# Kernel optimization log

Hardware: AMD Instinct MI355X
Metric: run time of the kernel (lower is better)

## Reference

```python
import jax, jax.numpy as jnp
import numpy as np

B, N, C, H = 4, 4096, 512, 16  # batch, seq (=input_resolution), dim, num_heads


def setup_inputs() -> dict:
    key = jax.random.key(0)
    k1, k2, k3, k4 = jax.random.split(key, 4)
    x = jax.random.normal(k1, (B, N, C), jnp.float32)
    Wqk = jax.random.normal(k2, (C, 2 * C), jnp.float32) / np.sqrt(C)
    bqk = jnp.zeros((2 * C,), jnp.float32)
    lepe_w = jax.random.normal(k3, (C, 1, 3), jnp.float32) * 0.1  # depthwise conv, groups=C
    lepe_b = jnp.zeros((C,), jnp.float32)
    return {"x": x, "Wqk": Wqk, "bqk": bqk, "lepe_w": lepe_w, "lepe_b": lepe_b}


def _rope(x):
    # x: [b, n, c]; 1D RoPE over the sequence axis, k_max = c // 2 pairs.
    b, n, c = x.shape
    k_max = c // 2
    theta = 1.0 / (10000.0 ** (jnp.arange(k_max, dtype=jnp.float32) / k_max))
    ang = jnp.arange(n, dtype=jnp.float32)[:, None] * theta  # [n, k_max]
    cos, sin = jnp.cos(ang), jnp.sin(ang)
    xr, xi = x[..., 0::2], x[..., 1::2]  # consecutive (re, im) pairs
    out = jnp.stack([xr * cos - xi * sin, xr * sin + xi * cos], axis=-1)
    return out.reshape(b, n, c)


def reference(x, Wqk, bqk, lepe_w, lepe_b):
    b, n, c = x.shape
    h = H
    d = c // h
    qk = x @ Wqk + bqk  # [b, n, 2c]
    q = jax.nn.elu(qk[..., :c]) + 1.0
    k = jax.nn.elu(qk[..., c:]) + 1.0
    q_rope = _rope(q).reshape(b, n, h, d).transpose(0, 2, 1, 3)  # [b,h,n,d]
    k_rope = _rope(k).reshape(b, n, h, d).transpose(0, 2, 1, 3)
    qh = q.reshape(b, n, h, d).transpose(0, 2, 1, 3)
    kh = k.reshape(b, n, h, d).transpose(0, 2, 1, 3)
    v = x.reshape(b, n, h, d).transpose(0, 2, 1, 3)
    # normalizer z = 1 / (q . mean_n(k) + eps)
    kmean = kh.mean(axis=2)  # [b,h,d]
    z = 1.0 / (jnp.einsum('bhnd,bhd->bhn', qh, kmean) + 1e-6)  # [b,h,n]
    # kv = (k_rope^T / sqrt(n)) @ (v / sqrt(n))
    kv = jnp.einsum('bhnd,bhne->bhde', k_rope, v) / n  # [b,h,d,d]
    out = jnp.einsum('bhnd,bhde->bhne', q_rope, kv) * z[..., None]  # [b,h,n,d]
    out = out.transpose(0, 2, 1, 3).reshape(b, n, c)
    # LePE: depthwise conv1d over sequence on v (v reassembled == x)
    vt = x.transpose(0, 2, 1)  # [b, c, n]
    lepe = jax.lax.conv_general_dilated(
        vt, lepe_w, window_strides=(1,), padding=((1, 1),),
        feature_group_count=c, dimension_numbers=('NCH', 'OIH', 'NCH'))
    lepe = lepe + lepe_b[None, :, None]
    return out + lepe.transpose(0, 2, 1)
```

## Files before the change

kernel.cpp:

```cpp
#include <hip/hip_runtime.h>

typedef unsigned short u16;
typedef u16   u16x8 __attribute__((ext_vector_type(8)));
typedef short s16x8 __attribute__((ext_vector_type(8)));
typedef float f32x4 __attribute__((ext_vector_type(4)));

__device__ __forceinline__ float b2f(u16 u) {
    return __uint_as_float(((unsigned)u) << 16);
}
__device__ __forceinline__ u16 f2b(float f) {
    unsigned x = __float_as_uint(f);
    x += 0x7fffu + ((x >> 16) & 1u);
    return (u16)(x >> 16);
}
__device__ __forceinline__ void gload_lds(const u16* g, u16* l) {
    __builtin_amdgcn_global_load_lds(
        (const __attribute__((address_space(1))) unsigned int*)g,
        (__attribute__((address_space(3))) unsigned int*)l, 16, 0, 0);
}

#define THETA_SCALE 0.05190512648261f

__global__ __launch_bounds__(256)
void k_prep(const float* __restrict__ X, u16* __restrict__ Xb,
            const float* __restrict__ W, u16* __restrict__ WT,
            float* __restrict__ kvz) {
    if (blockIdx.x < 4096) {
        size_t i = (size_t)(blockIdx.x * 256 + threadIdx.x) * 8;
        float4 a = *(const float4*)(X + i);
        float4 b = *(const float4*)(X + i + 4);
        u16x8 r;
        r[0] = f2b(a.x); r[1] = f2b(a.y); r[2] = f2b(a.z); r[3] = f2b(a.w);
        r[4] = f2b(b.x); r[5] = f2b(b.y); r[6] = f2b(b.z); r[7] = f2b(b.w);
        *(u16x8*)(Xb + i) = r;
    } else if (blockIdx.x < 4608) {
        __shared__ float tile[32][33];
        int bid = blockIdx.x - 4096;
        int c0 = (bid & 31) * 32;
        int r0 = (bid >> 5) * 32;
        int tx = threadIdx.x & 31;
        int ty = threadIdx.x >> 5;
        #pragma unroll
        for (int i = 0; i < 4; ++i) {
            int r = ty + i * 8;
            tile[r][tx] = W[(size_t)(r0 + r) * 1024 + c0 + tx];
        }
        __syncthreads();
        #pragma unroll
        for (int i = 0; i < 4; ++i) {
            int r = ty + i * 8;
            WT[(size_t)(c0 + r) * 512 + r0 + tx] = f2b(tile[tx][r]);
        }
    } else {
        size_t i = (size_t)(blockIdx.x - 4608) * 1024 + threadIdx.x * 4;
        *(float4*)(kvz + i) = make_float4(0.f, 0.f, 0.f, 0.f);
    }
}

__global__ __launch_bounds__(256)
void k_gemm(const u16* __restrict__ Xb, const u16* __restrict__ WT,
            const float* __restrict__ bqk,
            u16* __restrict__ Qb, u16* __restrict__ Kb) {
    __shared__ u16 As[128 * 64];
    __shared__ u16 Bs[128 * 64];
    const int t = threadIdx.x;
    const int m0 = blockIdx.x * 128;
    const int n0 = blockIdx.y * 128;
    const int lane = t & 63;
    const int wave = t >> 6;
    const int wm = (wave >> 1) * 64;
    const int wn = (wave & 1) * 64;
    const int quad = lane >> 4;
    const int l16 = lane & 15;
    const int lr = lane >> 3;
    const int cg = ((lane & 7) ^ lr) * 8;

    f32x4 acc[4][4];
    f32x4 zero4 = {0.f, 0.f, 0.f, 0.f};
    #pragma unroll
    for (int i = 0; i < 4; ++i)
        #pragma unroll
        for (int j = 0; j < 4; ++j) acc[i][j] = zero4;

    for (int k0 = 0; k0 < 512; k0 += 64) {
        __syncthreads();
        #pragma unroll
        for (int g = 0; g < 4; ++g) {
            int r0 = wave * 32 + g * 8;
            size_t ga = (size_t)(m0 + r0 + lr) * 512 + k0 + cg;
            size_t gb = (size_t)(n0 + r0 + lr) * 512 + k0 + cg;
            gload_lds(Xb + ga, &As[r0 * 64]);
            gload_lds(WT + gb, &Bs[r0 * 64]);
        }
        __syncthreads();
        #pragma unroll
        for (int ks = 0; ks < 64; ks += 32) {
            const int cbase = quad + (ks >> 3);
            s16x8 a4[4], b4[4];
            #pragma unroll
            for (int i = 0; i < 4; ++i) {
                int row = wm + i * 16 + l16;
                a4[i] = *(const s16x8*)&As[row * 64 + ((cbase ^ (row & 7)) * 8)];
            }
            #pragma unroll
            for (int j = 0; j < 4; ++j) {
                int row = wn + j * 16 + l16;
                b4[j] = *(const s16x8*)&Bs[row * 64 + ((cbase ^ (row & 7)) * 8)];
            }
            #pragma unroll
            for (int i = 0; i < 4; ++i)
                #pragma unroll
                for (int j = 0; j < 4; ++j)
                    acc[i][j] = __builtin_amdgcn_mfma_f32_16x16x32_bf16(
                        a4[i], b4[j], acc[i][j], 0, 0, 0);
        }
    }

    u16* O = (n0 < 512) ? Qb : Kb;
    #pragma unroll
    for (int i = 0; i < 4; ++i)
        #pragma unroll
        for (int j = 0; j < 4; ++j) {
            int col = n0 + wn + j * 16 + l16;
            float bias = bqk[col];
            int gc = col & 511;
            #pragma unroll
            for (int r = 0; r < 4; ++r) {
                int grow = m0 + wm + i * 16 + quad * 4 + r;
                float v = acc[i][j][r] + bias;
                v = v > 0.f ? v + 1.f : __expf(v);
                O[(size_t)grow * 512 + gc] = f2b(v);
            }
        }
}

__global__ __launch_bounds__(256)
void k_kv(const u16* __restrict__ Kb, const u16* __restrict__ Xb,
          float* __restrict__ kvbuf, float* __restrict__ ksum) {
    const int bh = blockIdx.x;
    const int b = bh >> 4, h = bh & 15;
    const int nb = blockIdx.y * 512;
    __shared__ u16 krT[32 * 72];
    __shared__ u16 vT[32 * 72];
    __shared__ float red[64 * 36];
    const int t = threadIdx.x;
    const int row = t >> 2;
    const int c8 = (t & 3) * 8;
    const int rot_w = 16 * ((c8 >> 3) & 3);
    const int lane = t & 63;
    const int wave = t >> 6;
    const int quad = lane >> 4;
    const int l16 = lane & 15;
    const int dq = (wave >> 1) * 16;
    const int eq = (wave & 1) * 16;
    const int ca = dq + l16;
    const int cb2 = eq + l16;
    const int rot_a = 16 * ((ca >> 3) & 3);
    const int rot_b = 16 * ((cb2 >> 3) & 3);

    float ksl[8] = {0, 0, 0, 0, 0, 0, 0, 0};
    f32x4 acc = {0.f, 0.f, 0.f, 0.f};

    float th[4];
    #pragma unroll
    for (int p = 0; p < 4; ++p)
        th[p] = exp2f(-THETA_SCALE * (float)(h * 16 + (c8 >> 1) + p));

    for (int pass = 0; pass < 8; ++pass) {
        int n = nb + pass * 64 + row;
        size_t base = (size_t)(b * 4096 + n) * 512 + h * 32 + c8;
        u16x8 k8 = *(const u16x8*)(Kb + base);
        u16x8 v8 = *(const u16x8*)(Xb + base);
        float kf[8], kr[8];
        #pragma unroll
        for (int j = 0; j < 8; ++j) kf[j] = b2f(k8[j]);
        #pragma unroll
        for (int p = 0; p < 4; ++p) {
            float sv, cv;
            sincosf((float)n * th[p], &sv, &cv);
            kr[2 * p]     = kf[2 * p] * cv - kf[2 * p + 1] * sv;
            kr[2 * p + 1] = kf[2 * p] * sv + kf[2 * p + 1] * cv;
        }
        #pragma unroll
        for (int j = 0; j < 8; ++j) ksl[j] += kf[j];
        if (pass) __syncthreads();
        int colw = (row + rot_w) & 63;
        #pragma unroll
        for (int j = 0; j < 8; ++j) {
            krT[(c8 + j) * 72 + colw] = f2b(kr[j]);
            vT[(c8 + j) * 72 + colw] = v8[j];
        }
        __syncthreads();
        #pragma unroll
        for (int ks = 0; ks < 64; ks += 32) {
            s16x8 a4 = *(const s16x8*)&krT[ca * 72 + ((ks + quad * 8 + rot_a) & 63)];
            s16x8 b4 = *(const s16x8*)&vT[cb2 * 72 + ((ks + quad * 8 + rot_b) & 63)];
            acc = __builtin_amdgcn_mfma_f32_16x16x32_bf16(a4, b4, acc, 0, 0, 0);
        }
    }

    #pragma unroll
    for (int r = 0; r < 4; ++r)
        atomicAdd(&kvbuf[(size_t)bh * 1024 + (dq + quad * 4 + r) * 32 + eq + l16],
                  acc[r]);

    __syncthreads();
    *(float4*)&red[row * 36 + c8]     = make_float4(ksl[0], ksl[1], ksl[2], ksl[3]);
    *(float4*)&red[row * 36 + c8 + 4] = make_float4(ksl[4], ksl[5], ksl[6], ksl[7]);
    __syncthreads();
    if (t < 32) {
        float s = 0.f;
        for (int r = 0; r < 64; ++r) s += red[r * 36 + t];
        atomicAdd(&ksum[bh * 32 + t], s);
    }
}

__global__ __launch_bounds__(256)
void k_out(const u16* __restrict__ Qb, const u16* __restrict__ Xb,
           const float* __restrict__ kvbuf, const float* __restrict__ ksum,
           const float* __restrict__ lw, const float* __restrict__ lb,
           float* __restrict__ OUT) {
    const int b = blockIdx.x >> 6;
    const int nb = (blockIdx.x & 63) * 64;
    const int hbase = blockIdx.y * 4;
    __shared__ u16 kvT_s[32 * 36];
    __shared__ u16 qr_s[64 * 36];
    __shared__ float out_s[64 * 36];
    __shared__ float ks_s[32];
    __shared__ float z_s[64];
    const int t = threadIdx.x;
    const int row = t >> 2;
    const int c4 = t & 3;
    const int e0 = c4 * 8;
    const int lane = t & 63;
    const int wave = t >> 6;
    const int quad = lane >> 4;
    const int l16 = lane & 15;
    const float invN = 1.f / 4096.f;
    const int n = nb + row;
    const size_t rowbase = (size_t)(b * 4096 + n) * 512;

    for (int hh = 0; hh < 4; ++hh) {
        const int h = hbase + hh;
        const int bh = b * 16 + h;
        if (hh) __syncthreads();
        {
            int id = t * 4;
            float4 kvv = *(const float4*)&kvbuf[(size_t)bh * 1024 + id];
            int d = id >> 5, e = id & 31;
            kvT_s[(e + 0) * 36 + d] = f2b(kvv.x * invN);
            kvT_s[(e + 1) * 36 + d] = f2b(kvv.y * invN);
            kvT_s[(e + 2) * 36 + d] = f2b(kvv.z * invN);
            kvT_s[(e + 3) * 36 + d] = f2b(kvv.w * invN);
        }
        if (t < 32) ks_s[t] = ksum[bh * 32 + t] * invN;
        __syncthreads();

        u16x8 q8 = *(const u16x8*)(Qb + rowbase + h * 32 + e0);
        float qf[8];
        #pragma unroll
        for (int j = 0; j < 8; ++j) qf[j] = b2f(q8[j]);
        float part = 0.f;
        #pragma unroll
        for (int j = 0; j < 8; ++j) part += qf[j] * ks_s[e0 + j];
        u16x8 qr8;
        #pragma unroll
        for (int p = 0; p < 4; ++p) {
            float th = exp2f(-THETA_SCALE * (float)(h * 16 + c4 * 4 + p));
            float sv, cv;
            sincosf((float)n * th, &sv, &cv);
            qr8[2 * p]     = f2b(qf[2 * p] * cv - qf[2 * p + 1] * sv);
            qr8[2 * p + 1] = f2b(qf[2 * p] * sv + qf[2 * p + 1] * cv);
        }
        *(u16x8*)&qr_s[row * 36 + e0] = qr8;
        part += __shfl_xor(part, 1);
        part += __shfl_xor(part, 2);
        if (c4 == 0) z_s[row] = 1.f / (part + 1e-6f);
        __syncthreads();

        {
            f32x4 zero4 = {0.f, 0.f, 0.f, 0.f};
            s16x8 a4 = *(const s16x8*)&qr_s[(wave * 16 + l16) * 36 + quad * 8];
            #pragma unroll
            for (int et = 0; et < 2; ++et) {
                s16x8 b4 = *(const s16x8*)&kvT_s[(et * 16 + l16) * 36 + quad * 8];
                f32x4 cacc = __builtin_amdgcn_mfma_f32_16x16x32_bf16(
                    a4, b4, zero4, 0, 0, 0);
                #pragma unroll
                for (int r = 0; r < 4; ++r)
                    out_s[(wave * 16 + quad * 4 + r) * 36 + et * 16 + l16] = cacc[r];
            }
        }
        __syncthreads();

        const float z = z_s[row];
        float4 o0 = *(const float4*)&out_s[row * 36 + e0];
        float4 o1 = *(const float4*)&out_s[row * 36 + e0 + 4];
        float o[8] = {o0.x, o0.y, o0.z, o0.w, o1.x, o1.y, o1.z, o1.w};
        const int cb = h * 32 + e0;
        u16x8 xc = *(const u16x8*)(Xb + rowbase + cb);
        u16x8 xm = {0, 0, 0, 0, 0, 0, 0, 0};
        u16x8 xp = {0, 0, 0, 0, 0, 0, 0, 0};
        if (n > 0)    xm = *(const u16x8*)(Xb + rowbase - 512 + cb);
        if (n < 4095) xp = *(const u16x8*)(Xb + rowbase + 512 + cb);
        float rv[8];
        #pragma unroll
        for (int j = 0; j < 8; ++j) {
            int c = cb + j;
            float lep = b2f(xm[j]) * lw[c * 3] +
                        b2f(xc[j]) * lw[c * 3 + 1] +
                        b2f(xp[j]) * lw[c * 3 + 2] + lb[c];
            rv[j] = o[j] * z + lep;
        }
        float* Of = OUT + rowbase + cb;
        *(float4*)Of       = make_float4(rv[0], rv[1], rv[2], rv[3]);
        *(float4*)(Of + 4) = make_float4(rv[4], rv[5], rv[6], rv[7]);
    }
}

extern "C" void kernel_launch(void* const* d_in, const int* in_sizes, int n_in,
                              void* d_out, int out_size, void* d_ws, size_t ws_size,
                              hipStream_t stream) {
    const float* x   = (const float*)d_in[0];
    const float* Wqk = (const float*)d_in[1];
    const float* bqk = (const float*)d_in[2];
    const float* lw  = (const float*)d_in[3];
    const float* lb  = (const float*)d_in[4];
    float* out = (float*)d_out;

    char* w = (char*)d_ws;
    u16* Kb      = (u16*)w;   w += (size_t)16384 * 512 * 2;
    u16* Qb      = (u16*)w;   w += (size_t)16384 * 512 * 2;
    u16* Xb      = (u16*)w;   w += (size_t)16384 * 512 * 2;
    u16* WT      = (u16*)w;   w += (size_t)1024 * 512 * 2;
    float* kvbuf = (float*)w; w += (size_t)64 * 1024 * 4;
    float* ksum  = (float*)w;

    k_prep<<<4674, 256, 0, stream>>>(x, Xb, Wqk, WT, kvbuf);
    k_gemm<<<dim3(128, 8), 256, 0, stream>>>(Xb, WT, bqk, Qb, Kb);
    k_kv<<<dim3(64, 8), 256, 0, stream>>>(Kb, Xb, kvbuf, ksum);
    k_out<<<dim3(256, 4), 256, 0, stream>>>(Qb, Xb, kvbuf, ksum, lw, lb, out);
}
```

Measured before the change: 146.5 us.

## Enlarge QK GEMM tiles to 256x256 with double-buffered LDS prefetch

```diff
diff --git a/kernel.cpp b/kernel.cpp
--- a/kernel.cpp
+++ b/kernel.cpp
@@ -57,68 +57,90 @@
     }
 }
 
-__global__ __launch_bounds__(256)
+__global__ __launch_bounds__(512, 2)
 void k_gemm(const u16* __restrict__ Xb, const u16* __restrict__ WT,
             const float* __restrict__ bqk,
             u16* __restrict__ Qb, u16* __restrict__ Kb) {
-    __shared__ u16 As[128 * 64];
-    __shared__ u16 Bs[128 * 64];
+    __shared__ u16 As[2][256 * 64];
+    __shared__ u16 Bs[2][256 * 64];
     const int t = threadIdx.x;
-    const int m0 = blockIdx.x * 128;
-    const int n0 = blockIdx.y * 128;
+    const int m0 = blockIdx.x * 256;
+    const int n0 = blockIdx.y * 256;
     const int lane = t & 63;
     const int wave = t >> 6;
-    const int wm = (wave >> 1) * 64;
-    const int wn = (wave & 1) * 64;
+    const int wm = (wave >> 2) * 128;
+    const int wn = (wave & 3) * 64;
     const int quad = lane >> 4;
     const int l16 = lane & 15;
-    const int lr = lane >> 3;
-    const int cg = ((lane & 7) ^ lr) * 8;
-
-    f32x4 acc[4][4];
-    f32x4 zero4 = {0.f, 0.f, 0.f, 0.f};
-    #pragma unroll
-    for (int i = 0; i < 4; ++i)
-        #pragma unroll
-        for (int j = 0; j < 4; ++j) acc[i][j] = zero4;
-
-    for (int k0 = 0; k0 < 512; k0 += 64) {
-        __syncthreads();
-        #pragma unroll
-        for (int g = 0; g < 4; ++g) {
-            int r0 = wave * 32 + g * 8;
-            size_t ga = (size_t)(m0 + r0 + lr) * 512 + k0 + cg;
-            size_t gb = (size_t)(n0 + r0 + lr) * 512 + k0 + cg;
-            gload_lds(Xb + ga, &As[r0 * 64]);
-            gload_lds(WT + gb, &Bs[r0 * 64]);
-        }
-        __syncthreads();
-        #pragma unroll
-        for (int ks = 0; ks < 64; ks += 32) {
-            const int cbase = quad + (ks >> 3);
-            s16x8 a4[4], b4[4];
-            #pragma unroll
-            for (int i = 0; i < 4; ++i) {
-                int row = wm + i * 16 + l16;
-                a4[i] = *(const s16x8*)&As[row * 64 + ((cbase ^ (row & 7)) * 8)];
+    const int srow = lane >> 3;
+    const int skc  = lane & 7;
+
+    f32x4 acc[8][4];
+    #pragma unroll
+    for (int i = 0; i < 8; ++i)
+        #pragma unroll
+        for (int j = 0; j < 4; ++j) acc[i][j] = (f32x4){0.f, 0.f, 0.f, 0.f};
+
+    #pragma unroll
+    for (int c = 0; c < 4; ++c) {
+        int row = c * 64 + wave * 8 + srow;
+        int kcs = (skc ^ (row & 7)) * 8;
+        gload_lds(Xb + (size_t)(m0 + row) * 512 + kcs,
+                  &As[0][(c * 64 + wave * 8) * 64]);
+        gload_lds(WT + (size_t)(n0 + row) * 512 + kcs,
+                  &Bs[0][(c * 64 + wave * 8) * 64]);
+    }
+
+    for (int kt = 0; kt < 8; ++kt) {
+        const int cur = kt & 1;
+        if (kt < 7) {
+            const int k0 = (kt + 1) * 64;
+            #pragma unroll
+            for (int c = 0; c < 4; ++c) {
+                int row = c * 64 + wave * 8 + srow;
+                int kcs = (skc ^ (row & 7)) * 8;
+                gload_lds(Xb + (size_t)(m0 + row) * 512 + k0 + kcs,
+                          &As[cur ^ 1][(c * 64 + wave * 8) * 64]);
+                gload_lds(WT + (size_t)(n0 + row) * 512 + k0 + kcs,
+                          &Bs[cur ^ 1][(c * 64 + wave * 8) * 64]);
+            }
+            asm volatile("s_waitcnt vmcnt(8)" ::: "memory");
+        } else {
+            asm volatile("s_waitcnt vmcnt(0)" ::: "memory");
+        }
+        __builtin_amdgcn_s_barrier();
+        asm volatile("" ::: "memory");
+
+        #pragma unroll
+        for (int s = 0; s < 2; ++s) {
+            const int cb = s * 4 + quad;
+            s16x8 af[8], bf[4];
+            #pragma unroll
+            for (int f = 0; f < 8; ++f) {
+                int row = wm + f * 16 + l16;
+                af[f] = *(const s16x8*)&As[cur][row * 64 + ((cb ^ (row & 7)) * 8)];
             }
             #pragma unroll
             for (int j = 0; j < 4; ++j) {
                 int row = wn + j * 16 + l16;
-                b4[j] = *(const s16x8*)&Bs[row * 64 + ((cbase ^ (row & 7)) * 8)];
-            }
-            #pragma unroll
-            for (int i = 0; i < 4; ++i)
+                bf[j] = *(const s16x8*)&Bs[cur][row * 64 + ((cb ^ (row & 7)) * 8)];
+            }
+            __builtin_amdgcn_s_setprio(1);
+            #pragma unroll
+            for (int f = 0; f < 8; ++f)
                 #pragma unroll
                 for (int j = 0; j < 4; ++j)
-                    acc[i][j] = __builtin_amdgcn_mfma_f32_16x16x32_bf16(
-                        a4[i], b4[j], acc[i][j], 0, 0, 0);
-        }
+                    acc[f][j] = __builtin_amdgcn_mfma_f32_16x16x32_bf16(
+                        af[f], bf[j], acc[f][j], 0, 0, 0);
+            __builtin_amdgcn_s_setprio(0);
+        }
+        asm volatile("" ::: "memory");
+        __builtin_amdgcn_s_barrier();
     }
 
     u16* O = (n0 < 512) ? Qb : Kb;
     #pragma unroll
-    for (int i = 0; i < 4; ++i)
+    for (int f = 0; f < 8; ++f)
         #pragma unroll
         for (int j = 0; j < 4; ++j) {
             int col = n0 + wn + j * 16 + l16;
@@ -126,8 +148,8 @@
             int gc = col & 511;
             #pragma unroll
             for (int r = 0; r < 4; ++r) {
-                int grow = m0 + wm + i * 16 + quad * 4 + r;
-                float v = acc[i][j][r] + bias;
+                int grow = m0 + wm + f * 16 + quad * 4 + r;
+                float v = acc[f][j][r] + bias;
                 v = v > 0.f ? v + 1.f : __expf(v);
                 O[(size_t)grow * 512 + gc] = f2b(v);
             }
@@ -337,7 +359,7 @@
     float* ksum  = (float*)w;
 
     k_prep<<<4674, 256, 0, stream>>>(x, Xb, Wqk, WT, kvbuf);
-    k_gemm<<<dim3(128, 8), 256, 0, stream>>>(Xb, WT, bqk, Qb, Kb);
+    k_gemm<<<dim3(64, 4), 512, 0, stream>>>(Xb, WT, bqk, Qb, Kb);
     k_kv<<<dim3(64, 8), 256, 0, stream>>>(Kb, Xb, kvbuf, ksum);
     k_out<<<dim3(256, 4), 256, 0, stream>>>(Qb, Xb, kvbuf, ksum, lw, lb, out);
 }
```

After: 141.1 us. -3.6%, faster.
